# Kernel tuning notes

Hardware: AMD Instinct MI355X
Metric: run time of the kernel (lower is better)

The kernel has to match this reference:

```python
import jax, jax.numpy as jnp
import numpy as np

TAU = 1.0

def setup_inputs() -> dict:
    key = jax.random.key(0)
    k1, k2 = jax.random.split(key)
    b, t, n, e, top_k = 2, 64, 1024, 512, 256
    x = jax.random.normal(k1, (b, t, n, e), dtype=jnp.float32)
    # torch nn.Linear(embed_size, top_k): weight [top_k, e], bias [top_k]
    W = jax.random.normal(k2, (top_k, e), dtype=jnp.float32) * (1.0 / np.sqrt(e))
    b_bias = jnp.zeros((top_k,), dtype=jnp.float32)
    return {"x": x, "W": W, "b_bias": b_bias}

def reference(x, W, b_bias):
    b, t, n, e = x.shape
    x_flat = x.reshape(b, t * n, e)                 # [b, m, e], m = t*n
    scores = x_flat @ W.T + b_bias                  # [b, m, top_k]
    weights = jax.nn.softmax(scores / TAU, axis=1)  # softmax over token axis m
    # weighted-sum pooling for all top_k slots at once (replaces torch loop)
    selected = jnp.einsum('bmk,bme->bke', weights, x_flat)  # [b, top_k, e]
    return selected
```

## Files before the change

### kernel.cpp

```cpp
#include <hip/hip_runtime.h>
#include <stdint.h>

#define B_DIM 2
#define M_DIM 65536
#define E_DIM 512
#define K_DIM 256

typedef __bf16 bf16_t;
typedef __bf16 bf16x8 __attribute__((ext_vector_type(8)));
typedef float  f32x4  __attribute__((ext_vector_type(4)));

#define SWZ(r) (((r) + ((r) >> 2)) & 3)

typedef const __attribute__((address_space(1))) void* gas_ptr;
typedef __attribute__((address_space(3))) void* las_ptr;

__device__ __forceinline__ void async_load16(const void* g, void* l) {
    __builtin_amdgcn_global_load_lds((gas_ptr)g, (las_ptr)l, 16, 0, 0);
}

__device__ __forceinline__ unsigned short bf16_bits(float f) {
    return __builtin_bit_cast(unsigned short, (__bf16)f);
}
__device__ __forceinline__ unsigned int pack2(float lo, float hi) {
    return (unsigned int)bf16_bits(lo) | ((unsigned int)bf16_bits(hi) << 16);
}

__global__ __launch_bounds__(256) void cast_w(const float* __restrict__ W, bf16_t* __restrict__ Wb) {
    int idx = blockIdx.x * 256 + threadIdx.x;
    float4 v = ((const float4*)W)[idx];
    ((uint2*)Wb)[idx] = make_uint2(pack2(v.x, v.y), pack2(v.z, v.w));
}

__global__ __launch_bounds__(256) void gemm1_exp_t(const float* __restrict__ x, const bf16_t* __restrict__ Wb,
                                                   bf16_t* __restrict__ pb, float* __restrict__ psums,
                                                   bf16_t* __restrict__ xT) {
    int gid = blockIdx.x;
    int mt = gid & 1023;
    int b  = gid >> 10;
    int m0 = mt * 64;
    int t = threadIdx.x, lane = t & 63, w = t >> 6;

    __shared__ __align__(16) char smem[32768];
    bf16_t* Alds = (bf16_t*)smem;
    bf16_t* Blds = (bf16_t*)(smem + 16384);
    bf16_t* Elds = (bf16_t*)smem;

    const float* xb = x + ((size_t)b * M_DIM + m0) * E_DIM;

    f32x4 zero = {0.f, 0.f, 0.f, 0.f};
    f32x4 acc[4][4];
#pragma unroll
    for (int i = 0; i < 4; ++i)
#pragma unroll
        for (int j = 0; j < 4; ++j) acc[i][j] = zero;

    int bst_row = t >> 2, bst_gl = t & 3;
    int bst_ge  = bst_gl ^ SWZ(bst_row);
    const float* bsrc = xb + (size_t)bst_row * E_DIM + bst_ge * 8;

    int ecol = t >> 3, msub = t & 7;

    int q = lane >> 4, r15 = lane & 15;

    for (int ke = 0; ke < 16; ++ke) {
        int e0 = ke * 32;
#pragma unroll
        for (int is = 0; is < 4; ++is) {
            int c = is * 256 + t;
            int row = c >> 2, gl = c & 3;
            int ge = gl ^ SWZ(row);
            async_load16(Wb + (size_t)row * E_DIM + e0 + ge * 8, Alds + c * 8);
        }
        {
            const float4* f = (const float4*)(bsrc + e0);
            float4 a0 = f[0], a1 = f[1];
            uint4 w4 = make_uint4(pack2(a0.x, a0.y), pack2(a0.z, a0.w),
                                  pack2(a1.x, a1.y), pack2(a1.z, a1.w));
            *(uint4*)(Blds + bst_row * 32 + bst_gl * 8) = w4;
        }
        __syncthreads();

        bf16x8 af[4], bfr[4];
#pragma unroll
        for (int i = 0; i < 4; ++i) {
            int r = w * 64 + i * 16 + r15;
            af[i] = *(const bf16x8*)(Alds + r * 32 + ((q ^ SWZ(r)) * 8));
        }
#pragma unroll
        for (int j = 0; j < 4; ++j) {
            int r = j * 16 + r15;
            bfr[j] = *(const bf16x8*)(Blds + r * 32 + ((q ^ SWZ(r)) * 8));
        }
#pragma unroll
        for (int i = 0; i < 4; ++i)
#pragma unroll
            for (int j = 0; j < 4; ++j)
                acc[i][j] = __builtin_amdgcn_mfma_f32_16x16x32_bf16(af[i], bfr[j], acc[i][j], 0, 0, 0);

        {
            const unsigned short* Bs = (const unsigned short*)Blds;
            unsigned short vs[8];
#pragma unroll
            for (int mm = 0; mm < 8; ++mm) {
                int m = msub * 8 + mm;
                int g = (ecol >> 3) ^ SWZ(m);
                vs[mm] = Bs[m * 32 + g * 8 + (ecol & 7)];
            }
            uint4 u = make_uint4((unsigned)vs[0] | ((unsigned)vs[1] << 16),
                                 (unsigned)vs[2] | ((unsigned)vs[3] << 16),
                                 (unsigned)vs[4] | ((unsigned)vs[5] << 16),
                                 (unsigned)vs[6] | ((unsigned)vs[7] << 16));
            *(uint4*)(xT + ((size_t)(b * E_DIM + e0 + ecol)) * M_DIM + m0 + msub * 8) = u;
        }
        __syncthreads();
    }

    int cc = lane & 15;
    float ksum[4][4];
#pragma unroll
    for (int i = 0; i < 4; ++i)
#pragma unroll
        for (int p = 0; p < 4; ++p) ksum[i][p] = 0.f;

#pragma unroll
    for (int i = 0; i < 4; ++i) {
        int kr = w * 64 + i * 16 + q * 4;
#pragma unroll
        for (int j = 0; j < 4; ++j) {
            int colb = j * 16 + cc;
            int g = colb >> 3, off = colb & 7;
#pragma unroll
            for (int p = 0; p < 4; ++p) {
                float v = __expf(acc[i][j][p]);
                ksum[i][p] += v;
                int k = kr + p;
                Elds[k * 64 + ((g ^ (k & 7)) * 8) + off] = (bf16_t)v;
            }
        }
    }
#pragma unroll
    for (int mask = 1; mask < 16; mask <<= 1)
#pragma unroll
        for (int i = 0; i < 4; ++i)
#pragma unroll
            for (int p = 0; p < 4; ++p)
                ksum[i][p] += __shfl_xor(ksum[i][p], mask, 64);
    if (cc == 0) {
        float* pp = psums + ((size_t)b * 1024 + mt) * 256;
#pragma unroll
        for (int i = 0; i < 4; ++i)
#pragma unroll
            for (int p = 0; p < 4; ++p)
                pp[w * 64 + i * 16 + q * 4 + p] = ksum[i][p];
    }
    __syncthreads();

    {
        int k = t;
        const bf16_t* row = Elds + k * 64;
        uint4* dst = (uint4*)(pb + ((size_t)(b * K_DIM + k)) * M_DIM + m0);
#pragma unroll
        for (int g = 0; g < 8; ++g)
            dst[g] = *(const uint4*)(row + ((g ^ (k & 7)) * 8));
    }
}

__global__ __launch_bounds__(256) void gemm2(const bf16_t* __restrict__ pb, const bf16_t* __restrict__ xT,
                                             float* __restrict__ part) {
    int bid = blockIdx.x;
    int kt = bid & 1, et = (bid >> 1) & 3, ch = (bid >> 3) & 31, b = bid >> 8;
    int t = threadIdx.x, lane = t & 63, w = t >> 6;
    int wk = w & 1, we = w >> 1;

    __shared__ __align__(16) bf16_t Alds[128 * 32];
    __shared__ __align__(16) bf16_t Blds[128 * 32];

    const bf16_t* Ab = pb + ((size_t)(b * K_DIM + kt * 128)) * M_DIM + ch * 2048;
    const bf16_t* Bb = xT + ((size_t)(b * E_DIM + et * 128)) * M_DIM + ch * 2048;

    f32x4 zero = {0.f, 0.f, 0.f, 0.f};
    f32x4 acc[4][4];
#pragma unroll
    for (int i = 0; i < 4; ++i)
#pragma unroll
        for (int j = 0; j < 4; ++j) acc[i][j] = zero;

    for (int km = 0; km < 64; ++km) {
        int m0 = km * 32;
#pragma unroll
        for (int is = 0; is < 2; ++is) {
            int c = is * 256 + t;
            int row = c >> 2, gl = c & 3;
            int ge = gl ^ SWZ(row);
            async_load16(Ab + (size_t)row * M_DIM + m0 + ge * 8, Alds + c * 8);
            async_load16(Bb + (size_t)row * M_DIM + m0 + ge * 8, Blds + c * 8);
        }
        __syncthreads();

        bf16x8 af[4], bfr[4];
        int q = lane >> 4, r15 = lane & 15;
#pragma unroll
        for (int i = 0; i < 4; ++i) {
            int r = wk * 64 + i * 16 + r15;
            af[i] = *(const bf16x8*)(Alds + r * 32 + ((q ^ SWZ(r)) * 8));
        }
#pragma unroll
        for (int j = 0; j < 4; ++j) {
            int r = we * 64 + j * 16 + r15;
            bfr[j] = *(const bf16x8*)(Blds + r * 32 + ((q ^ SWZ(r)) * 8));
        }
#pragma unroll
        for (int i = 0; i < 4; ++i)
#pragma unroll
            for (int j = 0; j < 4; ++j)
                acc[i][j] = __builtin_amdgcn_mfma_f32_16x16x32_bf16(af[i], bfr[j], acc[i][j], 0, 0, 0);
        __syncthreads();
    }

    float* pp = part + (size_t)bid * 16384;
    int q = lane >> 4, cc = lane & 15;
#pragma unroll
    for (int i = 0; i < 4; ++i)
#pragma unroll
        for (int p = 0; p < 4; ++p) {
            int kl = wk * 64 + i * 16 + q * 4 + p;
#pragma unroll
            for (int j = 0; j < 4; ++j) {
                int el = we * 64 + j * 16 + cc;
                pp[kl * 128 + el] = acc[i][j][p];
            }
        }
}

__global__ __launch_bounds__(256) void reduce_out(const float* __restrict__ part, const float* __restrict__ psums,
                                                  float* __restrict__ out) {
    int bid = blockIdx.x;
    int ehalf = bid & 1, k = (bid >> 1) & 255, b = bid >> 9;
    int t = threadIdx.x, lane = t & 63;

    float cs = 0.f;
#pragma unroll
    for (int c = 0; c < 4; ++c) {
        int mt = c * 256 + t;
        cs += psums[((size_t)b * 1024 + mt) * 256 + k];
    }
#pragma unroll
    for (int mask = 1; mask < 64; mask <<= 1) cs += __shfl_xor(cs, mask, 64);
    __shared__ float cspart[4];
    if (lane == 0) cspart[t >> 6] = cs;
    __syncthreads();
    float colsum = (cspart[0] + cspart[1]) + (cspart[2] + cspart[3]);

    int e = ehalf * 256 + t;
    int kt = k >> 7, kl = k & 127, et = e >> 7, el = e & 127;
    float s = 0.f;
#pragma unroll
    for (int ch = 0; ch < 32; ++ch) {
        int bid2 = kt | (et << 1) | (ch << 3) | (b << 8);
        s += part[(size_t)bid2 * 16384 + kl * 128 + el];
    }
    out[((size_t)(b * 256 + k)) * 512 + e] = s / colsum;
}

extern "C" void kernel_launch(void* const* d_in, const int* in_sizes, int n_in,
                              void* d_out, int out_size, void* d_ws, size_t ws_size,
                              hipStream_t stream) {
    (void)in_sizes; (void)n_in; (void)out_size; (void)ws_size;
    const float* x = (const float*)d_in[0];
    const float* W = (const float*)d_in[1];

    char* ws = (char*)d_ws;
    bf16_t* xT    = (bf16_t*)ws;
    bf16_t* Wb    = (bf16_t*)(ws + 134217728);
    bf16_t* pb    = (bf16_t*)(ws + 134479872);
    float*  psums = (float*)(ws + 201588736);
    float*  part  = (float*)(ws + 203685888);
    float*  out   = (float*)d_out;

    cast_w<<<128, 256, 0, stream>>>(W, Wb);
    gemm1_exp_t<<<2048, 256, 0, stream>>>(x, Wb, pb, psums, xT);
    gemm2<<<512, 256, 0, stream>>>(pb, xT, part);
    reduce_out<<<1024, 256, 0, stream>>>(part, psums, out);
}
```

Measured before the change: 517.4 us.

## Double K-step depth to 64 with XOR-8 swizzle and coalesced transposed stores

Both GEMM kernels now stage 64-wide K slices per iteration instead of 32. This halves the number of barrier-separated iterations, and the LDS swizzle changes to a row&7 XOR over 8 segments. The xT transpose reads are staggered per lane to avoid LDS bank conflicts. The pb store is reorganized so 8 consecutive threads write one contiguous 128-byte row segment instead of each thread writing a whole row. The cost is more LDS per block (40KB in gemm1, 32KB in gemm2), which may lower occupancy.

```diff
diff --git a/kernel.cpp b/kernel.cpp
--- a/kernel.cpp
+++ b/kernel.cpp
@@ -9,8 +9,6 @@
 typedef __bf16 bf16_t;
 typedef __bf16 bf16x8 __attribute__((ext_vector_type(8)));
 typedef float  f32x4  __attribute__((ext_vector_type(4)));
-
-#define SWZ(r) (((r) + ((r) >> 2)) & 3)
 
 typedef const __attribute__((address_space(1))) void* gas_ptr;
 typedef __attribute__((address_space(3))) void* las_ptr;
@@ -41,9 +39,9 @@
     int m0 = mt * 64;
     int t = threadIdx.x, lane = t & 63, w = t >> 6;
 
-    __shared__ __align__(16) char smem[32768];
+    __shared__ __align__(16) char smem[40960];
     bf16_t* Alds = (bf16_t*)smem;
-    bf16_t* Blds = (bf16_t*)(smem + 16384);
+    bf16_t* Blds = (bf16_t*)(smem + 32768);
     bf16_t* Elds = (bf16_t*)smem;
 
     const float* xb = x + ((size_t)b * M_DIM + m0) * E_DIM;
@@ -55,63 +53,73 @@
 #pragma unroll
         for (int j = 0; j < 4; ++j) acc[i][j] = zero;
 
-    int bst_row = t >> 2, bst_gl = t & 3;
-    int bst_ge  = bst_gl ^ SWZ(bst_row);
-    const float* bsrc = xb + (size_t)bst_row * E_DIM + bst_ge * 8;
-
-    int ecol = t >> 3, msub = t & 7;
+    int bst_r = t >> 2, bst_s0 = t & 3;
 
     int q = lane >> 4, r15 = lane & 15;
 
-    for (int ke = 0; ke < 16; ++ke) {
-        int e0 = ke * 32;
-#pragma unroll
-        for (int is = 0; is < 4; ++is) {
+    for (int ke = 0; ke < 8; ++ke) {
+        int e0 = ke * 64;
+#pragma unroll
+        for (int is = 0; is < 8; ++is) {
             int c = is * 256 + t;
-            int row = c >> 2, gl = c & 3;
-            int ge = gl ^ SWZ(row);
+            int row = c >> 3, sl = c & 7;
+            int ge = sl ^ (row & 7);
             async_load16(Wb + (size_t)row * E_DIM + e0 + ge * 8, Alds + c * 8);
         }
-        {
-            const float4* f = (const float4*)(bsrc + e0);
+#pragma unroll
+        for (int sg = 0; sg < 2; ++sg) {
+            int sl = bst_s0 + sg * 4;
+            int ge = sl ^ (bst_r & 7);
+            const float4* f = (const float4*)(xb + (size_t)bst_r * E_DIM + e0 + ge * 8);
             float4 a0 = f[0], a1 = f[1];
-            uint4 w4 = make_uint4(pack2(a0.x, a0.y), pack2(a0.z, a0.w),
-                                  pack2(a1.x, a1.y), pack2(a1.z, a1.w));
-            *(uint4*)(Blds + bst_row * 32 + bst_gl * 8) = w4;
+            *(uint4*)(Blds + bst_r * 64 + sl * 8) =
+                make_uint4(pack2(a0.x, a0.y), pack2(a0.z, a0.w), pack2(a1.x, a1.y), pack2(a1.z, a1.w));
         }
         __syncthreads();
 
-        bf16x8 af[4], bfr[4];
-#pragma unroll
-        for (int i = 0; i < 4; ++i) {
-            int r = w * 64 + i * 16 + r15;
-            af[i] = *(const bf16x8*)(Alds + r * 32 + ((q ^ SWZ(r)) * 8));
-        }
-#pragma unroll
-        for (int j = 0; j < 4; ++j) {
-            int r = j * 16 + r15;
-            bfr[j] = *(const bf16x8*)(Blds + r * 32 + ((q ^ SWZ(r)) * 8));
-        }
-#pragma unroll
-        for (int i = 0; i < 4; ++i)
-#pragma unroll
-            for (int j = 0; j < 4; ++j)
-                acc[i][j] = __builtin_amdgcn_mfma_f32_16x16x32_bf16(af[i], bfr[j], acc[i][j], 0, 0, 0);
+#pragma unroll
+        for (int h = 0; h < 2; ++h) {
+            bf16x8 af[4], bfr[4];
+#pragma unroll
+            for (int i = 0; i < 4; ++i) {
+                int r = w * 64 + i * 16 + r15;
+                int sl = (h * 4 + q) ^ (r & 7);
+                af[i] = *(const bf16x8*)(Alds + r * 64 + sl * 8);
+            }
+#pragma unroll
+            for (int j = 0; j < 4; ++j) {
+                int r = j * 16 + r15;
+                int sl = (h * 4 + q) ^ (r & 7);
+                bfr[j] = *(const bf16x8*)(Blds + r * 64 + sl * 8);
+            }
+#pragma unroll
+            for (int i = 0; i < 4; ++i)
+#pragma unroll
+                for (int j = 0; j < 4; ++j)
+                    acc[i][j] = __builtin_amdgcn_mfma_f32_16x16x32_bf16(af[i], bfr[j], acc[i][j], 0, 0, 0);
+        }
 
         {
             const unsigned short* Bs = (const unsigned short*)Blds;
-            unsigned short vs[8];
-#pragma unroll
-            for (int mm = 0; mm < 8; ++mm) {
-                int m = msub * 8 + mm;
-                int g = (ecol >> 3) ^ SWZ(m);
-                vs[mm] = Bs[m * 32 + g * 8 + (ecol & 7)];
-            }
-            uint4 u = make_uint4((unsigned)vs[0] | ((unsigned)vs[1] << 16),
-                                 (unsigned)vs[2] | ((unsigned)vs[3] << 16),
-                                 (unsigned)vs[4] | ((unsigned)vs[5] << 16),
-                                 (unsigned)vs[6] | ((unsigned)vs[7] << 16));
-            *(uint4*)(xT + ((size_t)(b * E_DIM + e0 + ecol)) * M_DIM + m0 + msub * 8) = u;
+            int l7 = t & 7;
+            int mbase = l7 * 8;
+            int ebase = t >> 3;
+#pragma unroll
+            for (int p = 0; p < 2; ++p) {
+                int ecol = p * 32 + ebase;
+                unsigned short vs[8];
+#pragma unroll
+                for (int s = 0; s < 8; ++s) {
+                    int mmr = (s + l7) & 7;
+                    int sl = (ecol >> 3) ^ mmr;
+                    vs[mmr] = Bs[(mbase + mmr) * 64 + sl * 8 + (ecol & 7)];
+                }
+                uint4 u = make_uint4((unsigned)vs[0] | ((unsigned)vs[1] << 16),
+                                     (unsigned)vs[2] | ((unsigned)vs[3] << 16),
+                                     (unsigned)vs[4] | ((unsigned)vs[5] << 16),
+                                     (unsigned)vs[6] | ((unsigned)vs[7] << 16));
+                *(uint4*)(xT + ((size_t)(b * E_DIM + e0 + ecol)) * M_DIM + m0 + mbase) = u;
+            }
         }
         __syncthreads();
     }
@@ -157,12 +165,14 @@
     __syncthreads();
 
     {
-        int k = t;
-        const bf16_t* row = Elds + k * 64;
-        uint4* dst = (uint4*)(pb + ((size_t)(b * K_DIM + k)) * M_DIM + m0);
-#pragma unroll
-        for (int g = 0; g < 8; ++g)
-            dst[g] = *(const uint4*)(row + ((g ^ (k & 7)) * 8));
+        int g = t & 7, rsub = t >> 3;
+        uint4* dstb = (uint4*)(pb + (size_t)b * K_DIM * M_DIM + m0);
+#pragma unroll
+        for (int p = 0; p < 8; ++p) {
+            int k = p * 32 + rsub;
+            uint4 u = *(const uint4*)(Elds + k * 64 + ((g ^ (k & 7)) * 8));
+            dstb[((size_t)k * M_DIM + g * 8) >> 3] = u;
+        }
     }
 }
 
@@ -173,8 +183,8 @@
     int t = threadIdx.x, lane = t & 63, w = t >> 6;
     int wk = w & 1, we = w >> 1;
 
-    __shared__ __align__(16) bf16_t Alds[128 * 32];
-    __shared__ __align__(16) bf16_t Blds[128 * 32];
+    __shared__ __align__(16) bf16_t Alds[128 * 64];
+    __shared__ __align__(16) bf16_t Blds[128 * 64];
 
     const bf16_t* Ab = pb + ((size_t)(b * K_DIM + kt * 128)) * M_DIM + ch * 2048;
     const bf16_t* Bb = xT + ((size_t)(b * E_DIM + et * 128)) * M_DIM + ch * 2048;
@@ -186,40 +196,46 @@
 #pragma unroll
         for (int j = 0; j < 4; ++j) acc[i][j] = zero;
 
-    for (int km = 0; km < 64; ++km) {
-        int m0 = km * 32;
-#pragma unroll
-        for (int is = 0; is < 2; ++is) {
+    int q = lane >> 4, r15 = lane & 15;
+
+    for (int km = 0; km < 32; ++km) {
+        int m0 = km * 64;
+#pragma unroll
+        for (int is = 0; is < 4; ++is) {
             int c = is * 256 + t;
-            int row = c >> 2, gl = c & 3;
-            int ge = gl ^ SWZ(row);
+            int row = c >> 3, sl = c & 7;
+            int ge = sl ^ (row & 7);
             async_load16(Ab + (size_t)row * M_DIM + m0 + ge * 8, Alds + c * 8);
             async_load16(Bb + (size_t)row * M_DIM + m0 + ge * 8, Blds + c * 8);
         }
         __syncthreads();
 
-        bf16x8 af[4], bfr[4];
-        int q = lane >> 4, r15 = lane & 15;
-#pragma unroll
-        for (int i = 0; i < 4; ++i) {
-            int r = wk * 64 + i * 16 + r15;
-            af[i] = *(const bf16x8*)(Alds + r * 32 + ((q ^ SWZ(r)) * 8));
-        }
-#pragma unroll
-        for (int j = 0; j < 4; ++j) {
-            int r = we * 64 + j * 16 + r15;
-            bfr[j] = *(const bf16x8*)(Blds + r * 32 + ((q ^ SWZ(r)) * 8));
-        }
-#pragma unroll
-        for (int i = 0; i < 4; ++i)
-#pragma unroll
-            for (int j = 0; j < 4; ++j)
-                acc[i][j] = __builtin_amdgcn_mfma_f32_16x16x32_bf16(af[i], bfr[j], acc[i][j], 0, 0, 0);
+#pragma unroll
+        for (int h = 0; h < 2; ++h) {
+            bf16x8 af[4], bfr[4];
+#pragma unroll
+            for (int i = 0; i < 4; ++i) {
+                int r = wk * 64 + i * 16 + r15;
+                int sl = (h * 4 + q) ^ (r & 7);
+                af[i] = *(const bf16x8*)(Alds + r * 64 + sl * 8);
+            }
+#pragma unroll
+            for (int j = 0; j < 4; ++j) {
+                int r = we * 64 + j * 16 + r15;
+                int sl = (h * 4 + q) ^ (r & 7);
+                bfr[j] = *(const bf16x8*)(Blds + r * 64 + sl * 8);
+            }
+#pragma unroll
+            for (int i = 0; i < 4; ++i)
+#pragma unroll
+                for (int j = 0; j < 4; ++j)
+                    acc[i][j] = __builtin_amdgcn_mfma_f32_16x16x32_bf16(af[i], bfr[j], acc[i][j], 0, 0, 0);
+        }
         __syncthreads();
     }
 
     float* pp = part + (size_t)bid * 16384;
-    int q = lane >> 4, cc = lane & 15;
+    int cc = lane & 15;
 #pragma unroll
     for (int i = 0; i < 4; ++i)
 #pragma unroll
```

Result: faster. 486.9 us (-5.9%).
